# Kernel optimization log

Hardware: AMD Instinct MI355X
Metric: run time of the kernel (lower is better)

The kernel has to match this reference:

```python
import jax, jax.numpy as jnp
import numpy as np

B, S, D, H = 4, 2048, 1024, 16
HD = D // H

def setup_inputs() -> dict:
    key = jax.random.key(0)
    ks = jax.random.split(key, 10)
    s = 1.0 / np.sqrt(D)
    inp = {
        'x': jax.random.normal(ks[0], (B, S, D), dtype=jnp.float32),
        'attention_mask': jnp.ones((B, S), dtype=jnp.int32),
        'Wq': jax.random.uniform(ks[1], (D, D), jnp.float32, -s, s),
        'bq': jax.random.uniform(ks[2], (D,), jnp.float32, -s, s),
        'Wk': jax.random.uniform(ks[3], (D, D), jnp.float32, -s, s),
        'bk': jax.random.uniform(ks[4], (D,), jnp.float32, -s, s),
        'Wv': jax.random.uniform(ks[5], (D, D), jnp.float32, -s, s),
        'bv': jax.random.uniform(ks[6], (D,), jnp.float32, -s, s),
        'Wo': jax.random.uniform(ks[7], (D, D), jnp.float32, -s, s),
        'bo': jax.random.uniform(ks[8], (D,), jnp.float32, -s, s),
    }
    return inp

def reference(x, Wq, bq, Wk, bk, Wv, bv, Wo, bo, attention_mask):
    scale = HD ** -0.5
    # torch Linear: y = x @ W^T + b
    def proj(W, b):
        return (x @ W.T + b).reshape(B, S, H, HD).transpose(0, 2, 1, 3)  # [B,H,S,hd]
    q = proj(Wq, bq)
    k = proj(Wk, bk)
    v = proj(Wv, bv)
    scores = jnp.einsum('bhqd,bhkd->bhqk', q, k) * scale  # [B,H,S,S]
    causal = jnp.triu(jnp.ones((S, S), dtype=bool), k=1)
    scores = jnp.where(causal, -jnp.inf, scores)
    pad = (attention_mask == 0)[:, None, None, :]  # [B,1,1,S]
    scores = jnp.where(pad, jnp.float32(-1e9), scores)
    probs = jax.nn.softmax(scores, axis=-1)
    out = jnp.einsum('bhqk,bhkd->bhqd', probs, v)  # [B,H,S,hd]
    out = out.transpose(0, 2, 1, 3).reshape(B, S, D)
    return out @ Wo.T + bo
```

## Files before the change

kernel.cpp:

```cpp
#include <hip/hip_runtime.h>
#include <hip/hip_bf16.h>

typedef unsigned short u16;
typedef float f32x4 __attribute__((ext_vector_type(4)));
typedef __bf16 bf16x8 __attribute__((ext_vector_type(8)));

#define BB 4
#define SS 2048
#define DD 1024
#define HH 16
#define HDD 64
#define MM (BB*SS)

__device__ __forceinline__ u16 f2bf(float f){
    union { float f; unsigned int i; } v; v.f = f;
    unsigned int i = v.i;
    return (u16)((i + 0x7FFFu + ((i >> 16) & 1u)) >> 16);
}
__device__ __forceinline__ ushort2 pk2(float a, float b){
    union { __hip_bfloat162 h; ushort2 u; } v;
    float2 t; t.x = a; t.y = b;
    v.h = __float22bfloat162_rn(t);
    return v.u;
}
__device__ __forceinline__ ushort4 pk4(float a, float b, float c, float d){
    ushort2 lo = pk2(a, b), hi = pk2(c, d);
    ushort4 r; r.x = lo.x; r.y = lo.y; r.z = hi.x; r.w = hi.y;
    return r;
}
__device__ __forceinline__ void gl2lds16(const void* g, void* l){
    __builtin_amdgcn_global_load_lds(
        (const __attribute__((address_space(1))) void*)g,
        (__attribute__((address_space(3))) void*)l, 16, 0, 0);
}

__device__ __forceinline__ void cvt8(const float* __restrict__ src,
                                     u16* __restrict__ dst, size_t i)
{
    const float4 a = *(const float4*)&src[i];
    const float4 b = *(const float4*)&src[i + 4];
    ushort4 lo = pk4(a.x, a.y, a.z, a.w);
    ushort4 hi = pk4(b.x, b.y, b.z, b.w);
    uint4 o;
    o.x = (unsigned)lo.x | ((unsigned)lo.y << 16);
    o.y = (unsigned)lo.z | ((unsigned)lo.w << 16);
    o.z = (unsigned)hi.x | ((unsigned)hi.y << 16);
    o.w = (unsigned)hi.z | ((unsigned)hi.w << 16);
    *(uint4*)&dst[i] = o;
}

__global__ __launch_bounds__(256) void cvt_k(const float* __restrict__ src,
                                             u16* __restrict__ dst)
{
    const size_t i = ((size_t)blockIdx.x * 256 + threadIdx.x) * 8;
    cvt8(src, dst, i);
}

__global__ __launch_bounds__(256) void cvtw3_k(
    const float* __restrict__ W0, const float* __restrict__ W1,
    const float* __restrict__ W2, u16* __restrict__ dst)
{
    const float* src = blockIdx.y == 0 ? W0 : (blockIdx.y == 1 ? W1 : W2);
    u16* d = dst + (size_t)blockIdx.y * (size_t)DD * DD;
    const size_t i = ((size_t)blockIdx.x * 256 + threadIdx.x) * 8;
    cvt8(src, d, i);
}

__global__ __launch_bounds__(256) void cvtw1_k(const float* __restrict__ W,
                                               u16* __restrict__ dst)
{
    const size_t i = ((size_t)blockIdx.x * 256 + threadIdx.x) * 8;
    cvt8(W, dst, i);
}

__device__ __forceinline__ void gemm_core(const u16* __restrict__ A,
                                          const u16* __restrict__ Wb,
                                          f32x4 (&acc)[4][4],
                                          u16 (&At)[2][128 * 32],
                                          u16 (&Bt)[2][128 * 32],
                                          int m0, int n0, int tid)
{
    const int lane = tid & 63, w = tid >> 6;
    const int quad = lane >> 4, l15 = lane & 15;
    const int wm = w >> 1, wn = w & 1;
    const int arow = lane >> 2;
    const int acol = (lane & 3) * 8;

    auto STG = [&](int bi, int kt) {
        const int kk = kt * 32;
        #pragma unroll
        for (int c = 0; c < 2; ++c) {
            const int ch = w * 2 + c;
            gl2lds16(&A [(size_t)(m0 + ch * 16 + arow) * DD + kk + acol], &At[bi][ch * 512]);
            gl2lds16(&Wb[(size_t)(n0 + ch * 16 + arow) * DD + kk + acol], &Bt[bi][ch * 512]);
        }
    };
    auto CMP = [&](int bi) {
        bf16x8 af[4], bfr[4];
        #pragma unroll
        for (int i = 0; i < 4; ++i)
            af[i] = *(const bf16x8*)&At[bi][(wm * 64 + i * 16 + l15) * 32 + quad * 8];
        #pragma unroll
        for (int j = 0; j < 4; ++j)
            bfr[j] = *(const bf16x8*)&Bt[bi][(wn * 64 + j * 16 + l15) * 32 + quad * 8];
        #pragma unroll
        for (int i = 0; i < 4; ++i)
            #pragma unroll
            for (int j = 0; j < 4; ++j)
                acc[i][j] = __builtin_amdgcn_mfma_f32_16x16x32_bf16(af[i], bfr[j], acc[i][j], 0, 0, 0);
    };

    STG(0, 0);
    __syncthreads();
    #pragma unroll 1
    for (int i = 0; i < 15; ++i) {
        STG(1, 2 * i + 1);
        CMP(0);
        __syncthreads();
        STG(0, 2 * i + 2);
        CMP(1);
        __syncthreads();
    }
    STG(1, 31);
    CMP(0);
    __syncthreads();
    CMP(1);
}

__device__ __forceinline__ void xcd_map(int bid, int& m0, int& n0){
    const int xcd = bid & 7, q = bid >> 3;
    m0 = (xcd * 8 + (q & 7)) * 128;
    n0 = (q >> 3) * 128;
}

__global__ __launch_bounds__(256, 4) void gemm_qkv_k(
    const u16* __restrict__ x,
    const float* __restrict__ bq, const float* __restrict__ bk,
    const float* __restrict__ bv,
    const u16* __restrict__ Wqb, const u16* __restrict__ Wkb,
    const u16* __restrict__ Wvb,
    u16* __restrict__ Q, u16* __restrict__ K, u16* __restrict__ V)
{
    __shared__ alignas(16) u16 At[2][128 * 32];
    __shared__ alignas(16) u16 Bt[2][128 * 32];
    const int tid = threadIdx.x, lane = tid & 63, w = tid >> 6;
    const int quad = lane >> 4, l15 = lane & 15;
    const int wm = w >> 1, wn = w & 1;
    const int z = blockIdx.y;
    const u16* Wmb = z == 0 ? Wqb : (z == 1 ? Wkb : Wvb);
    const float* bias = z == 0 ? bq : (z == 1 ? bk : bv);
    u16* Out = z == 0 ? Q : (z == 1 ? K : V);
    int m0, n0;
    xcd_map(blockIdx.x, m0, n0);

    f32x4 acc[4][4];
    #pragma unroll
    for (int i = 0; i < 4; ++i)
        #pragma unroll
        for (int j = 0; j < 4; ++j) acc[i][j] = (f32x4)(0.0f);

    gemm_core(x, Wmb, acc, At, Bt, m0, n0, tid);

    float bs[4];
    #pragma unroll
    for (int j = 0; j < 4; ++j) bs[j] = bias[n0 + wn * 64 + j * 16 + l15];

    const int b = m0 / SS;
    const int h = (n0 + wn * 64) / HDD;
    const size_t base = ((size_t)(b * HH + h)) * SS * HDD;
    #pragma unroll
    for (int i = 0; i < 4; ++i) {
        #pragma unroll
        for (int r = 0; r < 4; ++r) {
            const int s = (m0 % SS) + wm * 64 + i * 16 + quad * 4 + r;
            #pragma unroll
            for (int j = 0; j < 4; ++j) {
                const int hd = j * 16 + l15;
                Out[base + (size_t)s * HDD + hd] = f2bf(acc[i][j][r] + bs[j]);
            }
        }
    }
}

__global__ __launch_bounds__(256, 4) void gemm_out_k(
    const u16* __restrict__ A, const float* __restrict__ bo,
    const u16* __restrict__ Wob, float* __restrict__ Out)
{
    __shared__ alignas(16) u16 At[2][128 * 32];
    __shared__ alignas(16) u16 Bt[2][128 * 32];
    const int tid = threadIdx.x, lane = tid & 63, w = tid >> 6;
    const int quad = lane >> 4, l15 = lane & 15;
    const int wm = w >> 1, wn = w & 1;
    int m0, n0;
    xcd_map(blockIdx.x, m0, n0);

    f32x4 acc[4][4];
    #pragma unroll
    for (int i = 0; i < 4; ++i)
        #pragma unroll
        for (int j = 0; j < 4; ++j) acc[i][j] = (f32x4)(0.0f);

    gemm_core(A, Wob, acc, At, Bt, m0, n0, tid);

    float bs[4];
    #pragma unroll
    for (int j = 0; j < 4; ++j) bs[j] = bo[n0 + wn * 64 + j * 16 + l15];

    #pragma unroll
    for (int i = 0; i < 4; ++i) {
        #pragma unroll
        for (int r = 0; r < 4; ++r) {
            const int m = m0 + wm * 64 + i * 16 + quad * 4 + r;
            #pragma unroll
            for (int j = 0; j < 4; ++j) {
                const int n = n0 + wn * 64 + j * 16 + l15;
                Out[(size_t)m * DD + n] = acc[i][j][r] + bs[j];
            }
        }
    }
}

#define QT 256
#define KT 64
#define LDPV 66

#define LOG2E 1.4426950408889634f

__device__ __forceinline__ int swz128(int row, int bcol){
    return row * 128 + (bcol ^ ((row & 7) << 4));
}

__global__ __launch_bounds__(512, 3) void attn_k(
    const u16* __restrict__ Q, const u16* __restrict__ K,
    const u16* __restrict__ V, const int* __restrict__ mask,
    u16* __restrict__ AO)
{
    __shared__ alignas(16) u16 QPs[QT * 64];
    __shared__ alignas(16) u16 Ks[KT * 64];
    __shared__ alignas(16) u16 Vs[HDD * LDPV];
    __shared__ float padf[KT];

    const int tid = threadIdx.x, lane = tid & 63, w = tid >> 6;
    const int quad = lane >> 4, l15 = lane & 15;
    const int bh = blockIdx.x;
    const int y = blockIdx.y;
    const int qt = (y < 4) ? (7 - y) : (y - 4);
    const int b = bh >> 4, h = bh & 15;
    const int q0 = qt * QT;
    const size_t hoff = (size_t)bh * SS * HDD;
    const u16* Qh = Q + hoff;
    const u16* Kh = K + hoff;
    const u16* Vh = V + hoff;
    const int nkt = (q0 + QT) / KT;
    const float scale2 = 0.125f * LOG2E;
    const int wrow_end = q0 + w * 32 + 32;

    const int kslot = w * 64 + lane;
    const int krow = kslot >> 3;
    const int kbcol = ((kslot & 7) << 4) ^ ((krow & 7) << 4);

    for (int c = tid; c < QT * 8; c += 512) {
        const int row = c >> 3, cc = c & 7;
        *(uint4*)((char*)QPs + swz128(row, cc * 16)) =
            *(const uint4*)&Qh[(size_t)(q0 + row) * HDD + cc * 8];
    }
    __syncthreads();

    bf16x8 bQ[2][2];
    #pragma unroll
    for (int j = 0; j < 2; ++j)
        #pragma unroll
        for (int ks = 0; ks < 2; ++ks)
            bQ[j][ks] = *(const bf16x8*)((const char*)QPs +
                swz128(w * 32 + j * 16 + l15, ks * 64 + quad * 16));

    float m_run[2] = { -1e30f, -1e30f };
    float l_run[2] = { 0.f, 0.f };
    f32x4 o[4][2];
    #pragma unroll
    for (int i = 0; i < 4; ++i)
        #pragma unroll
        for (int j = 0; j < 2; ++j) o[i][j] = (f32x4)(0.0f);

    for (int kt = 0; kt < nkt; ++kt) {
        const int kt0 = kt * KT;
        __syncthreads();

        gl2lds16((const char*)Kh + (size_t)(kt0 + krow) * 128 + kbcol,
                 (char*)Ks + w * 1024);

        if (tid < 256) {
            const int kp = tid >> 3;
            const int c0 = (tid & 7) * 8;
            uint4 r0 = *(const uint4*)&Vh[(size_t)(kt0 + kp * 2 + 0) * HDD + c0];
            uint4 r1 = *(const uint4*)&Vh[(size_t)(kt0 + kp * 2 + 1) * HDD + c0];
            const u16* e0 = (const u16*)&r0;
            const u16* e1 = (const u16*)&r1;
            #pragma unroll
            for (int e = 0; e < 8; ++e) {
                ushort2 pkv; pkv.x = e0[e]; pkv.y = e1[e];
                *(ushort2*)&Vs[(c0 + e) * LDPV + kp * 2] = pkv;
            }
        } else if (tid < 320) {
            const int t = tid - 256;
            padf[t] = (mask[b * SS + kt0 + t] == 0) ? -1e9f : 0.0f;
        }
        __syncthreads();

        if (kt0 < wrow_end) {
        f32x4 sc[4][2];
        #pragma unroll
        for (int i = 0; i < 4; ++i)
            #pragma unroll
            for (int j = 0; j < 2; ++j) sc[i][j] = (f32x4)(0.0f);
        __builtin_amdgcn_s_setprio(1);
        #pragma unroll
        for (int ks = 0; ks < 2; ++ks) {
            bf16x8 aK[4];
            #pragma unroll
            for (int i = 0; i < 4; ++i)
                aK[i] = *(const bf16x8*)((const char*)Ks +
                    swz128(i * 16 + l15, ks * 64 + quad * 16));
            #pragma unroll
            for (int i = 0; i < 4; ++i)
                #pragma unroll
                for (int j = 0; j < 2; ++j)
                    sc[i][j] = __builtin_amdgcn_mfma_f32_16x16x32_bf16(aK[i], bQ[j][ks], sc[i][j], 0, 0, 0);
        }
        __builtin_amdgcn_s_setprio(0);

        f32x4 pb[4];
        #pragma unroll
        for (int i = 0; i < 4; ++i)
            pb[i] = *(const f32x4*)&padf[i * 16 + quad * 4];

        #pragma unroll
        for (int j = 0; j < 2; ++j) {
            const int qrow = q0 + w * 32 + j * 16 + l15;
            const bool needC = (kt0 + KT - 1) > (q0 + w * 32 + j * 16);
            float mx = -1e9f;
            if (needC) {
                #pragma unroll
                for (int i = 0; i < 4; ++i)
                    #pragma unroll
                    for (int r = 0; r < 4; ++r) {
                        const int kpg = kt0 + i * 16 + quad * 4 + r;
                        float s = fmaf(sc[i][j][r], scale2, pb[i][r]);
                        s = (kpg > qrow) ? -1e9f : s;
                        sc[i][j][r] = s; mx = fmaxf(mx, s);
                    }
            } else {
                #pragma unroll
                for (int i = 0; i < 4; ++i)
                    #pragma unroll
                    for (int r = 0; r < 4; ++r) {
                        float s = fmaf(sc[i][j][r], scale2, pb[i][r]);
                        sc[i][j][r] = s; mx = fmaxf(mx, s);
                    }
            }
            mx = fmaxf(mx, __shfl_xor(mx, 16, 64));
            mx = fmaxf(mx, __shfl_xor(mx, 32, 64));
            float nm = m_run[j];
            if (!__all(mx <= nm + 8.f)) {
                nm = fmaxf(nm, mx);
                const float alpha = __builtin_exp2f(m_run[j] - nm);
                m_run[j] = nm;
                l_run[j] *= alpha;
                #pragma unroll
                for (int i = 0; i < 4; ++i)
                    #pragma unroll
                    for (int r = 0; r < 4; ++r) o[i][j][r] *= alpha;
            }
            float rs = 0.f;
            #pragma unroll
            for (int i = 0; i < 4; ++i) {
                float p0 = __builtin_exp2f(sc[i][j][0] - nm);
                float p1 = __builtin_exp2f(sc[i][j][1] - nm);
                float p2 = __builtin_exp2f(sc[i][j][2] - nm);
                float p3 = __builtin_exp2f(sc[i][j][3] - nm);
                rs += (p0 + p1) + (p2 + p3);
                *(ushort4*)((char*)QPs + swz128(w * 32 + j * 16 + l15, i * 32 + quad * 8)) =
                    pk4(p0, p1, p2, p3);
            }
            l_run[j] += rs;
        }
        asm volatile("s_waitcnt lgkmcnt(0)" ::: "memory");

        __builtin_amdgcn_s_setprio(1);
        #pragma unroll
        for (int ks = 0; ks < 2; ++ks) {
            bf16x8 aV[4], bP[2];
            #pragma unroll
            for (int i = 0; i < 4; ++i)
                aV[i] = *(const bf16x8*)&Vs[(i * 16 + l15) * LDPV + ks * 32 + quad * 8];
            #pragma unroll
            for (int j = 0; j < 2; ++j)
                bP[j] = *(const bf16x8*)((const char*)QPs +
                    swz128(w * 32 + j * 16 + l15, ks * 64 + quad * 16));
            #pragma unroll
            for (int i = 0; i < 4; ++i)
                #pragma unroll
                for (int j = 0; j < 2; ++j)
                    o[i][j] = __builtin_amdgcn_mfma_f32_16x16x32_bf16(aV[i], bP[j], o[i][j], 0, 0, 0);
        }
        __builtin_amdgcn_s_setprio(0);
        }
    }

    #pragma unroll
    for (int j = 0; j < 2; ++j) {
        float l = l_run[j];
        l += __shfl_xor(l, 16, 64);
        l += __shfl_xor(l, 32, 64);
        const float inv = (l > 0.f) ? (1.f / l) : 0.f;
        const int s = q0 + w * 32 + j * 16 + l15;
        const size_t rb = ((size_t)(b * SS + s)) * DD + h * HDD;
        #pragma unroll
        for (int i = 0; i < 4; ++i)
            *(ushort4*)&AO[rb + i * 16 + quad * 4] =
                pk4(o[i][j][0] * inv, o[i][j][1] * inv, o[i][j][2] * inv, o[i][j][3] * inv);
    }
}

extern "C" void kernel_launch(void* const* d_in, const int* in_sizes, int n_in,
                              void* d_out, int out_size, void* d_ws, size_t ws_size,
                              hipStream_t stream)
{
    const float* x  = (const float*)d_in[0];
    const int* mask = (const int*)d_in[1];
    const float* Wq = (const float*)d_in[2];
    const float* bq = (const float*)d_in[3];
    const float* Wk = (const float*)d_in[4];
    const float* bk = (const float*)d_in[5];
    const float* Wv = (const float*)d_in[6];
    const float* bv = (const float*)d_in[7];
    const float* Wo = (const float*)d_in[8];
    const float* bo = (const float*)d_in[9];
    float* out = (float*)d_out;

    u16* ws = (u16*)d_ws;
    const size_t NE = (size_t)MM * DD;
    const size_t WE = (size_t)DD * DD;
    if (ws_size < 4 * NE * sizeof(u16)) return;

    u16* Qb = ws;
    u16* Kb = ws + NE;
    u16* Vb = ws + 2 * NE;
    u16* Ab = ws + 3 * NE;

    u16* Wscr = (u16*)d_out;

    dim3 blk(256);
    cvt_k<<<dim3(NE / 2048), blk, 0, stream>>>(x, Ab);
    cvtw3_k<<<dim3(WE / 2048, 3), blk, 0, stream>>>(Wq, Wk, Wv, Wscr);
    gemm_qkv_k<<<dim3(512, 3), blk, 0, stream>>>(
        Ab, bq, bk, bv, Wscr, Wscr + WE, Wscr + 2 * WE, Qb, Kb, Vb);
    attn_k<<<dim3(BB * HH, SS / QT), dim3(512), 0, stream>>>(Qb, Kb, Vb, mask, Ab);
    cvtw1_k<<<dim3(WE / 2048), blk, 0, stream>>>(Wo, Qb);
    gemm_out_k<<<dim3(512), blk, 0, stream>>>(Ab, bo, Qb, out);
}
```

Baseline: 315.9 us.

## Use 256x128 GEMM tiles with swapped operands and vectorized epilogue stores

```diff
diff --git a/kernel.cpp b/kernel.cpp
--- a/kernel.cpp
+++ b/kernel.cpp
@@ -73,36 +73,42 @@
     cvt8(W, dst, i);
 }
 
-__device__ __forceinline__ void gemm_core(const u16* __restrict__ A,
-                                          const u16* __restrict__ Wb,
+__device__ __forceinline__ void gemm_core(const u16* __restrict__ Wb,
+                                          const u16* __restrict__ Act,
                                           f32x4 (&acc)[4][4],
-                                          u16 (&At)[2][128 * 32],
+                                          u16 (&At)[2][256 * 32],
                                           u16 (&Bt)[2][128 * 32],
-                                          int m0, int n0, int tid)
+                                          int n0, int m0, int tid)
 {
     const int lane = tid & 63, w = tid >> 6;
     const int quad = lane >> 4, l15 = lane & 15;
-    const int wm = w >> 1, wn = w & 1;
+    const int wn2 = w & 3, wm2 = w >> 2;
     const int arow = lane >> 2;
     const int acol = (lane & 3) * 8;
 
     auto STG = [&](int bi, int kt) {
         const int kk = kt * 32;
         #pragma unroll
-        for (int c = 0; c < 2; ++c) {
-            const int ch = w * 2 + c;
-            gl2lds16(&A [(size_t)(m0 + ch * 16 + arow) * DD + kk + acol], &At[bi][ch * 512]);
-            gl2lds16(&Wb[(size_t)(n0 + ch * 16 + arow) * DD + kk + acol], &Bt[bi][ch * 512]);
+        for (int c0 = 0; c0 < 3; ++c0) {
+            const int c = w * 3 + c0;
+            if (c < 16) {
+                gl2lds16(&Wb[(size_t)(n0 + c * 16 + arow) * DD + kk + acol],
+                         &At[bi][c * 512]);
+            } else {
+                const int cb = c - 16;
+                gl2lds16(&Act[(size_t)(m0 + cb * 16 + arow) * DD + kk + acol],
+                         &Bt[bi][cb * 512]);
+            }
         }
     };
     auto CMP = [&](int bi) {
         bf16x8 af[4], bfr[4];
         #pragma unroll
         for (int i = 0; i < 4; ++i)
-            af[i] = *(const bf16x8*)&At[bi][(wm * 64 + i * 16 + l15) * 32 + quad * 8];
+            af[i] = *(const bf16x8*)&At[bi][(wn2 * 64 + i * 16 + l15) * 32 + quad * 8];
         #pragma unroll
         for (int j = 0; j < 4; ++j)
-            bfr[j] = *(const bf16x8*)&Bt[bi][(wn * 64 + j * 16 + l15) * 32 + quad * 8];
+            bfr[j] = *(const bf16x8*)&Bt[bi][(wm2 * 64 + j * 16 + l15) * 32 + quad * 8];
         #pragma unroll
         for (int i = 0; i < 4; ++i)
             #pragma unroll
@@ -127,13 +133,7 @@
     CMP(1);
 }
 
-__device__ __forceinline__ void xcd_map(int bid, int& m0, int& n0){
-    const int xcd = bid & 7, q = bid >> 3;
-    m0 = (xcd * 8 + (q & 7)) * 128;
-    n0 = (q >> 3) * 128;
-}
-
-__global__ __launch_bounds__(256, 4) void gemm_qkv_k(
+__global__ __launch_bounds__(512, 2) void gemm_qkv_k(
     const u16* __restrict__ x,
     const float* __restrict__ bq, const float* __restrict__ bk,
     const float* __restrict__ bv,
@@ -141,17 +141,16 @@
     const u16* __restrict__ Wvb,
     u16* __restrict__ Q, u16* __restrict__ K, u16* __restrict__ V)
 {
-    __shared__ alignas(16) u16 At[2][128 * 32];
+    __shared__ alignas(16) u16 At[2][256 * 32];
     __shared__ alignas(16) u16 Bt[2][128 * 32];
     const int tid = threadIdx.x, lane = tid & 63, w = tid >> 6;
     const int quad = lane >> 4, l15 = lane & 15;
-    const int wm = w >> 1, wn = w & 1;
-    const int z = blockIdx.y;
+    const int wn2 = w & 3, wm2 = w >> 2;
+    const int z = blockIdx.z;
     const u16* Wmb = z == 0 ? Wqb : (z == 1 ? Wkb : Wvb);
     const float* bias = z == 0 ? bq : (z == 1 ? bk : bv);
     u16* Out = z == 0 ? Q : (z == 1 ? K : V);
-    int m0, n0;
-    xcd_map(blockIdx.x, m0, n0);
+    const int m0 = blockIdx.x * 128, n0 = blockIdx.y * 256;
 
     f32x4 acc[4][4];
     #pragma unroll
@@ -159,40 +158,38 @@
         #pragma unroll
         for (int j = 0; j < 4; ++j) acc[i][j] = (f32x4)(0.0f);
 
-    gemm_core(x, Wmb, acc, At, Bt, m0, n0, tid);
-
-    float bs[4];
-    #pragma unroll
-    for (int j = 0; j < 4; ++j) bs[j] = bias[n0 + wn * 64 + j * 16 + l15];
+    gemm_core(Wmb, x, acc, At, Bt, n0, m0, tid);
+
+    f32x4 bsv[4];
+    #pragma unroll
+    for (int i = 0; i < 4; ++i)
+        bsv[i] = *(const f32x4*)&bias[n0 + wn2 * 64 + i * 16 + quad * 4];
 
     const int b = m0 / SS;
-    const int h = (n0 + wn * 64) / HDD;
+    const int h = (n0 + wn2 * 64) / HDD;
     const size_t base = ((size_t)(b * HH + h)) * SS * HDD;
     #pragma unroll
-    for (int i = 0; i < 4; ++i) {
-        #pragma unroll
-        for (int r = 0; r < 4; ++r) {
-            const int s = (m0 % SS) + wm * 64 + i * 16 + quad * 4 + r;
-            #pragma unroll
-            for (int j = 0; j < 4; ++j) {
-                const int hd = j * 16 + l15;
-                Out[base + (size_t)s * HDD + hd] = f2bf(acc[i][j][r] + bs[j]);
-            }
-        }
-    }
-}
-
-__global__ __launch_bounds__(256, 4) void gemm_out_k(
+    for (int j = 0; j < 4; ++j) {
+        const int s = (m0 % SS) + wm2 * 64 + j * 16 + l15;
+        #pragma unroll
+        for (int i = 0; i < 4; ++i) {
+            *(ushort4*)&Out[base + (size_t)s * HDD + i * 16 + quad * 4] =
+                pk4(acc[i][j][0] + bsv[i][0], acc[i][j][1] + bsv[i][1],
+                    acc[i][j][2] + bsv[i][2], acc[i][j][3] + bsv[i][3]);
+        }
+    }
+}
+
+__global__ __launch_bounds__(512, 2) void gemm_out_k(
     const u16* __restrict__ A, const float* __restrict__ bo,
     const u16* __restrict__ Wob, float* __restrict__ Out)
 {
-    __shared__ alignas(16) u16 At[2][128 * 32];
+    __shared__ alignas(16) u16 At[2][256 * 32];
     __shared__ alignas(16) u16 Bt[2][128 * 32];
     const int tid = threadIdx.x, lane = tid & 63, w = tid >> 6;
     const int quad = lane >> 4, l15 = lane & 15;
-    const int wm = w >> 1, wn = w & 1;
-    int m0, n0;
-    xcd_map(blockIdx.x, m0, n0);
+    const int wn2 = w & 3, wm2 = w >> 2;
+    const int m0 = blockIdx.x * 128, n0 = blockIdx.y * 256;
 
     f32x4 acc[4][4];
     #pragma unroll
@@ -200,22 +197,24 @@
         #pragma unroll
         for (int j = 0; j < 4; ++j) acc[i][j] = (f32x4)(0.0f);
 
-    gemm_core(A, Wob, acc, At, Bt, m0, n0, tid);
-
-    float bs[4];
-    #pragma unroll
-    for (int j = 0; j < 4; ++j) bs[j] = bo[n0 + wn * 64 + j * 16 + l15];
-
-    #pragma unroll
-    for (int i = 0; i < 4; ++i) {
-        #pragma unroll
-        for (int r = 0; r < 4; ++r) {
-            const int m = m0 + wm * 64 + i * 16 + quad * 4 + r;
-            #pragma unroll
-            for (int j = 0; j < 4; ++j) {
-                const int n = n0 + wn * 64 + j * 16 + l15;
-                Out[(size_t)m * DD + n] = acc[i][j][r] + bs[j];
-            }
+    gemm_core(Wob, A, acc, At, Bt, n0, m0, tid);
+
+    f32x4 bsv[4];
+    #pragma unroll
+    for (int i = 0; i < 4; ++i)
+        bsv[i] = *(const f32x4*)&bo[n0 + wn2 * 64 + i * 16 + quad * 4];
+
+    #pragma unroll
+    for (int j = 0; j < 4; ++j) {
+        const int m = m0 + wm2 * 64 + j * 16 + l15;
+        #pragma unroll
+        for (int i = 0; i < 4; ++i) {
+            float4 f;
+            f.x = acc[i][j][0] + bsv[i][0];
+            f.y = acc[i][j][1] + bsv[i][1];
+            f.z = acc[i][j][2] + bsv[i][2];
+            f.w = acc[i][j][3] + bsv[i][3];
+            *(float4*)&Out[(size_t)m * DD + n0 + wn2 * 64 + i * 16 + quad * 4] = f;
         }
     }
 }
@@ -453,9 +452,9 @@
     dim3 blk(256);
     cvt_k<<<dim3(NE / 2048), blk, 0, stream>>>(x, Ab);
     cvtw3_k<<<dim3(WE / 2048, 3), blk, 0, stream>>>(Wq, Wk, Wv, Wscr);
-    gemm_qkv_k<<<dim3(512, 3), blk, 0, stream>>>(
+    gemm_qkv_k<<<dim3(MM / 128, DD / 256, 3), dim3(512), 0, stream>>>(
         Ab, bq, bk, bv, Wscr, Wscr + WE, Wscr + 2 * WE, Qb, Kb, Vb);
     attn_k<<<dim3(BB * HH, SS / QT), dim3(512), 0, stream>>>(Qb, Kb, Vb, mask, Ab);
     cvtw1_k<<<dim3(WE / 2048), blk, 0, stream>>>(Wo, Qb);
-    gemm_out_k<<<dim3(512), blk, 0, stream>>>(Ab, bo, Qb, out);
-}
+    gemm_out_k<<<dim3(MM / 128, DD / 256), dim3(512), 0, stream>>>(Ab, bo, Qb, out);
+}
```

Result: no change. 316.0 us (+0.0%).
